# Kernel optimization log

Hardware: AMD Instinct MI355X
Metric: run time of the kernel (lower is better)

Reference implementation:

```python
import jax, jax.numpy as jnp
import numpy as np

DIM = 1024
HEADS = 16
HEAD_DIM = DIM // HEADS
MLP_HID = 4 * DIM
LN_EPS = 1e-5


def layer_norm(x, g, b):
    mu = jnp.mean(x, axis=-1, keepdims=True)
    var = jnp.mean((x - mu) ** 2, axis=-1, keepdims=True)
    return (x - mu) * jax.lax.rsqrt(var + LN_EPS) * g + b


def setup_inputs() -> dict:
    key = jax.random.key(0)
    ks = jax.random.split(key, 8)
    s = 0.02
    return {
        "x": jax.random.normal(ks[0], (8, 1024, DIM), dtype=jnp.float32),
        "attention_mask": jnp.ones((8, 1024), dtype=jnp.int32),
        "ln1_g": jnp.ones((DIM,), jnp.float32),
        "ln1_b": jnp.zeros((DIM,), jnp.float32),
        "qkv_w": jax.random.normal(ks[1], (3 * DIM, DIM), jnp.float32) * s,
        "proj_w": jax.random.normal(ks[2], (DIM, DIM), jnp.float32) * s,
        "proj_b": jnp.zeros((DIM,), jnp.float32),
        "ln2_g": jnp.ones((DIM,), jnp.float32),
        "ln2_b": jnp.zeros((DIM,), jnp.float32),
        "fc1_w": jax.random.normal(ks[3], (MLP_HID, DIM), jnp.float32) * s,
        "fc1_b": jnp.zeros((MLP_HID,), jnp.float32),
        "fc2_w": jax.random.normal(ks[4], (DIM, MLP_HID), jnp.float32) * s,
        "fc2_b": jnp.zeros((DIM,), jnp.float32),
    }


def reference(x, attention_mask, ln1_g, ln1_b, qkv_w, proj_w, proj_b,
              ln2_g, ln2_b, fc1_w, fc1_b, fc2_w, fc2_b):
    B, N, C = x.shape
    scale = HEAD_DIM ** -0.5

    # --- attention branch ---
    h = layer_norm(x, ln1_g, ln1_b)
    qkv = h @ qkv_w.T                       # [B,N,3C] (no qkv bias)
    qkv = qkv.reshape(B, N, 3, HEADS, HEAD_DIM).transpose(2, 0, 3, 1, 4)
    q, k, v = qkv[0], qkv[1], qkv[2]        # each [B,H,N,Dh]
    attn = jnp.einsum('bhnd,bhmd->bhnm', q, k) * scale
    mask = (attention_mask == 0)[:, None, None, :]  # [B,1,1,N]
    attn = jnp.where(mask, -jnp.inf, attn)
    attn = jax.nn.softmax(attn, axis=-1)
    out = jnp.einsum('bhnm,bhmd->bhnd', attn, v)
    out = out.transpose(0, 2, 1, 3).reshape(B, N, C)
    out = out @ proj_w.T + proj_b
    x = x + out

    # --- MLP branch ---
    h = layer_norm(x, ln2_g, ln2_b)
    h = jax.nn.gelu(h @ fc1_w.T + fc1_b, approximate=False)
    h = h @ fc2_w.T + fc2_b
    return x + h
```

## Files before the change

kernel.cpp:

```cpp
#include <hip/hip_runtime.h>
#include <hip/hip_bf16.h>
#include <stdint.h>
#include <math.h>

#define DIMC 1024
#define SEQ 1024
#define NBATCH 8
#define NHEADS 16
#define HDIM 64
#define MLPHID 4096
#define NROWS (NBATCH*SEQ)

typedef __attribute__((ext_vector_type(8))) short short8;
typedef __attribute__((ext_vector_type(4))) float f32x4;
typedef __attribute__((ext_vector_type(16))) float f32x16;
typedef __attribute__((ext_vector_type(4))) unsigned int u32x4;

__device__ __forceinline__ short f2bf(float f) {
  union { float f; uint32_t u; } x; x.f = f;
  uint32_t r = (x.u + 0x7FFFu + ((x.u >> 16) & 1u)) >> 16;
  return (short)r;
}

__device__ __forceinline__ unsigned int cvtpk(float lo, float hi_) {
  unsigned int r;
  asm("v_cvt_pk_bf16_f32 %0, %1, %2" : "=v"(r) : "v"(lo), "v"(hi_));
  return r;
}

__device__ __forceinline__ float gelu_f(float v) {
  const float t = v * v;
  const float p = fmaf(t, 0.044715f, 1.0f);
  const float e = __builtin_amdgcn_exp2f(2.3022082f * v * p);
  return v - v * __builtin_amdgcn_rcpf(e + 1.0f);
}

__device__ __forceinline__ f32x4 mfma16(short8 a, short8 b, f32x4 c) {
  return __builtin_amdgcn_mfma_f32_16x16x32_bf16(a, b, c, 0, 0, 0);
}
__device__ __forceinline__ f32x16 mfma32(short8 a, short8 b, f32x16 c) {
  return __builtin_amdgcn_mfma_f32_32x32x16_bf16(a, b, c, 0, 0, 0);
}

__device__ __forceinline__ void gload16(const void* g, void* l) {
  __builtin_amdgcn_global_load_lds(
      (const __attribute__((address_space(1))) uint32_t*)g,
      (__attribute__((address_space(3))) uint32_t*)l, 16, 0, 0);
}

__global__ __launch_bounds__(256)
void f2bw_kernel(const float* __restrict__ w0, const float* __restrict__ w1,
                 const float* __restrict__ w2, const float* __restrict__ w3,
                 short* __restrict__ o0, short* __restrict__ o1,
                 short* __restrict__ o2, short* __restrict__ o3) {
  const int i = blockIdx.x * 256 + threadIdx.x;
  const float4* src;
  short4* dst;
  if (i < 786432)       { src = (const float4*)w0 + i;             dst = (short4*)o0 + i; }
  else if (i < 1048576) { src = (const float4*)w1 + (i - 786432);  dst = (short4*)o1 + (i - 786432); }
  else if (i < 2097152) { src = (const float4*)w2 + (i - 1048576); dst = (short4*)o2 + (i - 1048576); }
  else                  { src = (const float4*)w3 + (i - 2097152); dst = (short4*)o3 + (i - 2097152); }
  const float4 v = *src;
  short4 o;
  o.x = f2bf(v.x); o.y = f2bf(v.y); o.z = f2bf(v.z); o.w = f2bf(v.w);
  *dst = o;
}

__global__ __launch_bounds__(256)
void ln_kernel(const float* __restrict__ x, const float* __restrict__ g,
               const float* __restrict__ beta, short* __restrict__ out) {
  const int row = blockIdx.x;
  const int tid = threadIdx.x;
  const float4 v = ((const float4*)(x + (size_t)row * DIMC))[tid];
  float s = v.x + v.y + v.z + v.w;
  float q = v.x*v.x + v.y*v.y + v.z*v.z + v.w*v.w;
#pragma unroll
  for (int o = 32; o > 0; o >>= 1) { s += __shfl_down(s, o); q += __shfl_down(q, o); }
  __shared__ float rs[4], rq[4];
  const int lane = tid & 63, w = tid >> 6;
  if (lane == 0) { rs[w] = s; rq[w] = q; }
  __syncthreads();
  s = rs[0] + rs[1] + rs[2] + rs[3];
  q = rq[0] + rq[1] + rq[2] + rq[3];
  const float mean = s * (1.0f / DIMC);
  const float var = q * (1.0f / DIMC) - mean * mean;
  const float rstd = rsqrtf(var + 1e-5f);
  const float4 gv = ((const float4*)g)[tid];
  const float4 bv = ((const float4*)beta)[tid];
  short4 o4;
  o4.x = f2bf((v.x - mean) * rstd * gv.x + bv.x);
  o4.y = f2bf((v.y - mean) * rstd * gv.y + bv.y);
  o4.z = f2bf((v.z - mean) * rstd * gv.z + bv.z);
  o4.w = f2bf((v.w - mean) * rstd * gv.w + bv.w);
  ((short4*)(out + (size_t)row * DIMC))[tid] = o4;
}

#define NOVM ((void)0)
#define NOST ((void)0)
#define VMC4 asm volatile("s_waitcnt vmcnt(4)" ::: "memory")
#define VMC2 asm volatile("s_waitcnt vmcnt(2)" ::: "memory")

#define SA(DB, H, T) \
  gload16(sA0 + (H)*hstep + (size_t)(T)*64, stb + ((DB)*4 + (H))*16384); \
  gload16(sA1 + (H)*hstep + (size_t)(T)*64, stb + ((DB)*4 + (H))*16384 + 8192)

#define SB(DB, H, T) \
  gload16(sB0 + (H)*hstep + (size_t)(T)*64, stb + ((DB)*4 + 2 + (H))*16384); \
  gload16(sB1 + (H)*hstep + (size_t)(T)*64, stb + ((DB)*4 + 2 + (H))*16384 + 8192)

#define PH(DB, QA, QB, LDA, LDB, STAGE, VM) \
  do { \
    if (LDA) { \
      _Pragma("unroll") \
      for (int mi = 0; mi < 4; ++mi) { \
        _Pragma("unroll") \
        for (int ks = 0; ks < 2; ++ks) \
          af[mi][ks] = *(const short8*)(ard##DB + (((QA)*4 + mi)*2 + ks)*1024); \
      } \
    } \
    if (LDB) { \
      _Pragma("unroll") \
      for (int ni = 0; ni < 2; ++ni) { \
        _Pragma("unroll") \
        for (int ks = 0; ks < 2; ++ks) \
          bfv[QB][ni][ks] = *(const short8*)(brd##DB + (((QB)*2 + ni)*2 + ks)*1024); \
      } \
    } \
    STAGE; \
    __builtin_amdgcn_s_barrier(); \
    asm volatile("s_waitcnt lgkmcnt(0)" ::: "memory"); \
    __builtin_amdgcn_sched_barrier(0); \
    __builtin_amdgcn_s_setprio(1); \
    _Pragma("unroll") \
    for (int ks = 0; ks < 2; ++ks) { \
      _Pragma("unroll") \
      for (int mi = 0; mi < 4; ++mi) { \
        _Pragma("unroll") \
        for (int ni = 0; ni < 2; ++ni) \
          acc[(QA)*4 + mi][(QB)*2 + ni] = \
            mfma16(af[mi][ks], bfv[QB][ni][ks], acc[(QA)*4 + mi][(QB)*2 + ni]); \
      } \
    } \
    __builtin_amdgcn_s_setprio(0); \
    VM; \
    __builtin_amdgcn_s_barrier(); \
  } while (0)

template<bool BIAS, bool GELU, bool RESID, bool OBF16>
__global__ __launch_bounds__(512)
void gemm8p(const short* __restrict__ A, const short* __restrict__ W,
            const float* __restrict__ bias, const float* __restrict__ resid,
            float* __restrict__ outF, short* __restrict__ outB,
            int M, int N, int K, int ntl, int mt8)
{
  __shared__ __align__(16) char lsm[131072];
  const int tid = threadIdx.x;
  const int lane = tid & 63;
  const int w = tid >> 6;
  const int wm = w >> 2;
  const int wn = w & 3;
  const int fr = lane & 15;
  const int fko = (lane >> 4) << 3;

  const int bid = blockIdx.x;
  const int xcd = bid & 7, l = bid >> 3;
  const int bm = (xcd * mt8 + l / ntl) << 8;
  const int bn = (l % ntl) << 8;

  int row_[2], kk_[2];
#pragma unroll
  for (int j = 0; j < 2; ++j) {
    const int s = j * 8 + (tid >> 6);
    const int r16 = (tid & 63) >> 2;
    const int cb = ((tid & 3) << 4) ^ (((tid >> 5) & 1) << 5);
    row_[j] = (s >> 1) * 16 + r16;
    kk_[j]  = (s & 1) * 32 + (cb >> 1);
  }
  const short* sA0 = A + (size_t)(bm + row_[0]) * K + kk_[0];
  const short* sA1 = A + (size_t)(bm + row_[1]) * K + kk_[1];
  const short* sB0 = W + (size_t)(bn + row_[0]) * K + kk_[0];
  const short* sB1 = W + (size_t)(bn + row_[1]) * K + kk_[1];
  const size_t hstep = (size_t)128 * K;
  char* stb = lsm + tid * 16;

  const int lofs = fr * 64 + ((fko << 1) ^ (((fr >> 3) & 1) << 5));
  const char* ard0 = lsm + wm * 16384 + lofs;
  const char* brd0 = lsm + 32768 + (wn >> 1) * 16384 + (wn & 1) * 8192 + lofs;
  const char* ard1 = ard0 + 65536;
  const char* brd1 = brd0 + 65536;

  short8 af[4][2];
  short8 bfv[2][2][2];
  f32x4 acc[8][4] = {};

  SA(0, 0, 0); SA(0, 1, 0);
  SB(0, 0, 0); SB(0, 1, 0);
  SB(1, 0, 1); SB(1, 1, 1);
  VMC4;
  __builtin_amdgcn_s_barrier();

  const int nk = K >> 6;
  const int nit = nk >> 1;
  const int tmask = nk - 1;
  for (int it = 0; it < nit; ++it) {
    const int t1 = 2 * it + 1;
    const int t2 = (2 * it + 2) & tmask;
    const int t3 = (2 * it + 3) & tmask;
    PH(0, 0, 0, 1, 1, SA(1, 0, t1), NOVM);
    PH(0, 0, 1, 0, 1, SA(1, 1, t1), NOVM);
    PH(0, 1, 1, 1, 0, SB(0, 0, t2), NOVM);
    PH(0, 1, 0, 0, 0, SB(0, 1, t2), VMC4);
    PH(1, 0, 0, 1, 1, SA(0, 0, t2), NOVM);
    PH(1, 0, 1, 0, 1, SA(0, 1, t2), NOVM);
    PH(1, 1, 1, 1, 0, SB(1, 0, t3), NOVM);
    PH(1, 1, 0, 0, 0, SB(1, 1, t3), VMC4);
  }

  asm volatile("s_waitcnt vmcnt(0)" ::: "memory");
  __builtin_amdgcn_s_barrier();

  const int orow0 = bm + wm * 128 + ((lane >> 4) << 2);
  const int ocol0 = bn + wn * 64 + fr;
#pragma unroll
  for (int mi = 0; mi < 8; ++mi) {
#pragma unroll
    for (int r = 0; r < 4; ++r) {
      const int row = orow0 + mi * 16 + r;
      const size_t base = (size_t)row * N;
#pragma unroll
      for (int ni = 0; ni < 4; ++ni) {
        const int col = ocol0 + ni * 16;
        float v = acc[mi][ni][r];
        if (BIAS) v += bias[col];
        if (GELU) v = gelu_f(v);
        if (RESID) v += resid[base + col];
        if (OBF16) outB[base + col] = f2bf(v);
        else       outF[base + col] = v;
      }
    }
  }
}

#define SA2(DB, H, T) \
  gload16(sA0 + (H)*hstep + (size_t)(T)*64, stb + ((DB)*3 + (H))*16384); \
  gload16(sA1 + (H)*hstep + (size_t)(T)*64, stb + ((DB)*3 + (H))*16384 + 8192)

#define SB2(DB, T) \
  gload16(sB0 + (size_t)(T)*64, stb + ((DB)*3 + 2)*16384); \
  gload16(sB1 + (size_t)(T)*64, stb + ((DB)*3 + 2)*16384 + 8192)

#define PH2(DB, QA, QB, LDA, LDB, STAGE, VM) \
  do { \
    if (LDA) { \
      _Pragma("unroll") \
      for (int i = 0; i < 2; ++i) { \
        _Pragma("unroll") \
        for (int ks = 0; ks < 2; ++ks) \
          af[i][ks] = *(const short8*)(ard##DB + (((QA)*2 + i)*2 + ks)*1024); \
      } \
    } \
    if (LDB) { \
      _Pragma("unroll") \
      for (int jn = 0; jn < 2; ++jn) { \
        _Pragma("unroll") \
        for (int ks = 0; ks < 2; ++ks) \
          bfv[QB][jn][ks] = *(const short8*)(brd##DB + (((QB)*2 + jn)*2 + ks)*1024); \
      } \
    } \
    STAGE; \
    __builtin_amdgcn_s_barrier(); \
    asm volatile("s_waitcnt lgkmcnt(0)" ::: "memory"); \
    __builtin_amdgcn_sched_barrier(0); \
    __builtin_amdgcn_s_setprio(1); \
    _Pragma("unroll") \
    for (int ks = 0; ks < 2; ++ks) { \
      _Pragma("unroll") \
      for (int i = 0; i < 2; ++i) { \
        _Pragma("unroll") \
        for (int jn = 0; jn < 2; ++jn) \
          acc[(QA)*2 + i][(QB)*2 + jn] = \
            mfma16(af[i][ks], bfv[QB][jn][ks], acc[(QA)*2 + i][(QB)*2 + jn]); \
      } \
    } \
    __builtin_amdgcn_s_setprio(0); \
    VM; \
    __builtin_amdgcn_s_barrier(); \
  } while (0)

template<bool BIAS, bool GELU, bool RESID, bool OBF16, bool QSCALE>
__global__ __launch_bounds__(512)
void gemm8pn(const short* __restrict__ A, const short* __restrict__ W,
             const float* __restrict__ bias, const float* __restrict__ resid,
             float* __restrict__ outF, short* __restrict__ outB,
             int M, int N, int K, int ntl, int mt8)
{
  __shared__ __align__(16) char lsm[98304];
  const int tid = threadIdx.x;
  const int lane = tid & 63;
  const int w = tid >> 6;
  const int wm = w >> 1;
  const int wn = w & 1;
  const int fr = lane & 15;
  const int fko = (lane >> 4) << 3;

  const int bid = blockIdx.x;
  const int xcd = bid & 7, l = bid >> 3;
  const int bm = (xcd * mt8 + l / ntl) << 8;
  const int bn = (l % ntl) << 7;

  int row_[2], kk_[2];
#pragma unroll
  for (int j = 0; j < 2; ++j) {
    const int s = j * 8 + (tid >> 6);
    const int r16 = (tid & 63) >> 2;
    const int cb = ((tid & 3) << 4) ^ (((tid >> 5) & 1) << 5);
    row_[j] = (s >> 1) * 16 + r16;
    kk_[j]  = (s & 1) * 32 + (cb >> 1);
  }
  const short* sA0 = A + (size_t)(bm + row_[0]) * K + kk_[0];
  const short* sA1 = A + (size_t)(bm + row_[1]) * K + kk_[1];
  const short* sB0 = W + (size_t)(bn + row_[0]) * K + kk_[0];
  const short* sB1 = W + (size_t)(bn + row_[1]) * K + kk_[1];
  const size_t hstep = (size_t)128 * K;
  char* stb = lsm + tid * 16;

  const int lofs = fr * 64 + ((fko << 1) ^ (((fr >> 3) & 1) << 5));
  const char* ard0 = lsm + (wm >> 1) * 16384 + (wm & 1) * 8192 + lofs;
  const char* brd0 = lsm + 32768 + wn * 8192 + lofs;
  const char* ard1 = ard0 + 49152;
  const char* brd1 = brd0 + 49152;

  short8 af[2][2];
  short8 bfv[2][2][2];
  f32x4 acc[4][4] = {};

  SA2(0, 0, 0); SA2(0, 1, 0); SB2(0, 0);
  SB2(1, 1);
  VMC2;
  __builtin_amdgcn_s_barrier();

  const int nk = K >> 6;
  const int nit = nk >> 1;
  const int tmask = nk - 1;
  for (int it = 0; it < nit; ++it) {
    const int t1 = 2 * it + 1;
    const int t2 = (2 * it + 2) & tmask;
    const int t3 = (2 * it + 3) & tmask;
    PH2(0, 0, 0, 1, 1, SA2(1, 0, t1), NOVM);
    PH2(0, 0, 1, 0, 1, SA2(1, 1, t1), NOVM);
    PH2(0, 1, 1, 1, 0, SB2(0, t2),    NOVM);
    PH2(0, 1, 0, 0, 0, NOST,          VMC2);
    PH2(1, 0, 0, 1, 1, SA2(0, 0, t2), NOVM);
    PH2(1, 0, 1, 0, 1, SA2(0, 1, t2), NOVM);
    PH2(1, 1, 1, 1, 0, SB2(1, t3),    NOVM);
    PH2(1, 1, 0, 0, 0, NOST,          VMC2);
  }

  asm volatile("s_waitcnt vmcnt(0)" ::: "memory");
  __builtin_amdgcn_s_barrier();

  const int orow0 = bm + wm * 64 + ((lane >> 4) << 2);
  const int ocol0 = bn + wn * 64 + fr;
#pragma unroll
  for (int mi = 0; mi < 4; ++mi) {
#pragma unroll
    for (int r = 0; r < 4; ++r) {
      const int row = orow0 + mi * 16 + r;
      const size_t base = (size_t)row * N;
#pragma unroll
      for (int ni = 0; ni < 4; ++ni) {
        const int col = ocol0 + ni * 16;
        float v = acc[mi][ni][r];
        if (BIAS) v += bias[col];
        if (GELU) v = gelu_f(v);
        if (QSCALE) v *= (col < 1024 ? 0.18033688f : 1.0f);
        if (RESID) v += resid[base + col];
        if (OBF16) outB[base + col] = f2bf(v);
        else       outF[base + col] = v;
      }
    }
  }
}

__global__ __launch_bounds__(256)
void attn_kernel(const short* __restrict__ qkv, const int* __restrict__ amask,
                 short* __restrict__ out)
{
  __shared__ __align__(16) char lsm[36864];
  char* lsK = lsm;
  char* lsV = lsm + 16384;
  int* lmask = (int*)(lsm + 32768);
  __shared__ int anym;

  const int tid = threadIdx.x;
  const int lane = tid & 63;
  const int w = tid >> 6;
  const int l31 = lane & 31;
  const int hi = lane >> 5;
  const int swz = (l31 & 7) << 4;

  const int bid = blockIdx.x;
  const int swzb = ((bid & 7) << 7) | (bid >> 3);
  const int qt = swzb & 7;
  const int h = (swzb >> 3) & 15;
  const int b = swzb >> 7;
  const size_t rowbase = (size_t)b * SEQ;
  const short* qkvB = qkv + rowbase * 3072 + h * 64;

  const int4 mv = ((const int4*)(amask + b * SEQ))[tid];
  if (tid == 0) anym = 0;
  ((int4*)lmask)[tid] = mv;
  __syncthreads();
  if ((mv.x & mv.y & mv.z & mv.w) == 0) atomicOr(&anym, 1);

  const int q0 = qt * 128 + w * 32;
  const short* qptr = qkvB + (size_t)(q0 + l31) * 3072;
  short8 qf[4];
#pragma unroll
  for (int ks = 0; ks < 4; ++ks)
    qf[ks] = *(const short8*)(qptr + ks * 16 + hi * 8);

  const int krow = tid >> 3;
  const int kcc = (((tid & 7) * 16) ^ ((krow & 7) << 4)) >> 1;
  const short* gK = qkvB + 1024 + kcc;
  char* ldK = lsK + tid * 16;
  const int vr = tid & 63;
  const int vc0 = (tid >> 6) << 3;
  const short* gV = qkvB + 2048 + vc0;

  gload16(gK + (size_t)krow * 3072, ldK);
  gload16(gK + (size_t)(krow + 32) * 3072, ldK + 4096);
  {
    short8 a0 = *(const short8*)(gV + (size_t)vr * 3072);
    short8 a1 = *(const short8*)(gV + (size_t)vr * 3072 + 32);
#pragma unroll
    for (int j = 0; j < 8; ++j) {
      *(short*)(lsV + (vc0 + j) * 128 + ((2 * vr) ^ (j << 4))) = a0[j];
      *(short*)(lsV + (vc0 + 32 + j) * 128 + ((2 * vr) ^ (j << 4))) = a1[j];
    }
  }
  __syncthreads();

  f32x16 oacc[2] = {};
  float psum = 0.f;

  for (int c = 0; c < 16; ++c) {
    const int cur = c & 1;
    const char* lKc = lsK + cur * 8192;
    const char* lVc = lsV + cur * 8192;
    const bool pf = (c < 15);
    short8 vv0, vv1;
    if (pf) {
      const size_t nb_ = (size_t)(c + 1) * 64;
      char* ldKn = ldK + (cur ^ 1) * 8192;
      gload16(gK + (nb_ + krow) * 3072, ldKn);
      gload16(gK + (nb_ + krow + 32) * 3072, ldKn + 4096);
      vv0 = *(const short8*)(gV + (nb_ + vr) * 3072);
      vv1 = *(const short8*)(gV + (nb_ + vr) * 3072 + 32);
    }

    f32x16 pacc[2] = {};
    __builtin_amdgcn_s_setprio(1);
#pragma unroll
    for (int ks = 0; ks < 4; ++ks) {
#pragma unroll
      for (int s = 0; s < 2; ++s) {
        short8 kf = *(const short8*)(lKc + (s * 32 + l31) * 128 +
                                     ((ks * 32 + hi * 16) ^ swz));
        pacc[s] = mfma32(kf, qf[ks], pacc[s]);
      }
    }
    __builtin_amdgcn_s_setprio(0);

    if (pf) {
      char* lVn = lsV + (cur ^ 1) * 8192;
#pragma unroll
      for (int j = 0; j < 8; ++j) {
        *(short*)(lVn + (vc0 + j) * 128 + ((2 * vr) ^ (j << 4))) = vv0[j];
        *(short*)(lVn + (vc0 + 32 + j) * 128 + ((2 * vr) ^ (j << 4))) = vv1[j];
      }
    }

    if (anym) {
      const int kv0 = c * 64;
#pragma unroll
      for (int s = 0; s < 2; ++s)
#pragma unroll
        for (int r = 0; r < 16; ++r) {
          const int kv = kv0 + 32 * s + (r & 3) + 8 * (r >> 2) + 4 * hi;
          if (lmask[kv] == 0) pacc[s][r] = -1e30f;
        }
    }

    float pe[2][16];
#pragma unroll
    for (int s = 0; s < 2; ++s)
#pragma unroll
      for (int r = 0; r < 16; ++r) {
        const float p = __builtin_amdgcn_exp2f(pacc[s][r]);
        pe[s][r] = p;
        psum += p;
      }

    short8 pa[4];
#pragma unroll
    for (int ks = 0; ks < 4; ++ks) {
      const int sh = ks >> 1, kb = (ks & 1) << 3;
      unsigned int aa = cvtpk(pe[sh][kb + 0], pe[sh][kb + 1]);
      unsigned int bb = cvtpk(pe[sh][kb + 4], pe[sh][kb + 5]);
      unsigned int cc = cvtpk(pe[sh][kb + 2], pe[sh][kb + 3]);
      unsigned int dd = cvtpk(pe[sh][kb + 6], pe[sh][kb + 7]);
      asm volatile("v_permlane32_swap_b32 %0, %1" : "+v"(aa), "+v"(bb));
      asm volatile("v_permlane32_swap_b32 %0, %1" : "+v"(cc), "+v"(dd));
      u32x4 t;
      t[0] = aa; t[1] = cc; t[2] = bb; t[3] = dd;
      pa[ks] = __builtin_bit_cast(short8, t);
    }

    __builtin_amdgcn_s_setprio(1);
#pragma unroll
    for (int nb = 0; nb < 2; ++nb)
#pragma unroll
      for (int ks = 0; ks < 4; ++ks) {
        short8 vf = *(const short8*)(lVc + (nb * 32 + l31) * 128 +
                                     ((ks * 32 + hi * 16) ^ swz));
        oacc[nb] = mfma32(pa[ks], vf, oacc[nb]);
      }
    __builtin_amdgcn_s_setprio(0);

    __syncthreads();
  }

  const float lt = psum + __shfl_xor(psum, 32);
  const size_t orow = rowbase + q0;
#pragma unroll
  for (int r = 0; r < 16; ++r) {
    const int q = (r & 3) + 8 * (r >> 2) + 4 * hi;
    const float linv = 1.0f / __shfl(lt, q);
    short* op = out + (orow + q) * DIMC + h * 64 + l31;
    op[0]  = f2bf(oacc[0][r] * linv);
    op[32] = f2bf(oacc[1][r] * linv);
  }
}

extern "C" void kernel_launch(void* const* d_in, const int* in_sizes, int n_in,
                              void* d_out, int out_size, void* d_ws, size_t ws_size,
                              hipStream_t stream)
{
  const float* x      = (const float*)d_in[0];
  const int*   amask  = (const int*)d_in[1];
  const float* ln1_g  = (const float*)d_in[2];
  const float* ln1_b  = (const float*)d_in[3];
  const float* qkv_w  = (const float*)d_in[4];
  const float* proj_w = (const float*)d_in[5];
  const float* proj_b = (const float*)d_in[6];
  const float* ln2_g  = (const float*)d_in[7];
  const float* ln2_b  = (const float*)d_in[8];
  const float* fc1_w  = (const float*)d_in[9];
  const float* fc1_b  = (const float*)d_in[10];
  const float* fc2_w  = (const float*)d_in[11];
  const float* fc2_b  = (const float*)d_in[12];
  float* out = (float*)d_out;

  char* ws = (char*)d_ws;
  short* wqkv  = (short*)(ws);
  short* wproj = (short*)(ws + 6291456);
  short* wfc1  = (short*)(ws + 8388608);
  short* wfc2  = (short*)(ws + 16777216);
  float* x1    = (float*)(ws + 25165824);
  short* hb    = (short*)(ws + 58720256);
  short* qkvo  = (short*)(ws + 75497472);
  short* attno = (short*)(ws + 125829120);
  short* fc1o  = (short*)(ws + 75497472);

  f2bw_kernel<<<12288, 256, 0, stream>>>(qkv_w, proj_w, fc1_w, fc2_w,
                                         wqkv, wproj, wfc1, wfc2);

  ln_kernel<<<NROWS, 256, 0, stream>>>(x, ln1_g, ln1_b, hb);

  gemm8pn<false, false, false, true, true><<<768, 512, 0, stream>>>(
      hb, wqkv, nullptr, nullptr, nullptr, qkvo, NROWS, 3 * DIMC, DIMC, 24, 4);

  attn_kernel<<<1024, 256, 0, stream>>>(qkvo, amask, attno);

  gemm8pn<true, false, true, false, false><<<256, 512, 0, stream>>>(
      attno, wproj, proj_b, x, x1, nullptr, NROWS, DIMC, DIMC, 8, 4);

  ln_kernel<<<NROWS, 256, 0, stream>>>(x1, ln2_g, ln2_b, hb);

  gemm8p<true, true, false, true><<<512, 512, 0, stream>>>(
      hb, wfc1, fc1_b, nullptr, nullptr, fc1o, NROWS, MLPHID, DIMC, 16, 4);

  gemm8pn<true, false, true, false, false><<<256, 512, 0, stream>>>(
      fc1o, wfc2, fc2_b, x1, out, nullptr, NROWS, DIMC, MLPHID, 8, 4);
}
```

Before: 327.1 us.

## Deepen B-tile prefetch in gemm8pn and use it for fc1

Reworks the 256x128 GEMM pipeline so the B operand is staged into four rotating LDS buffers, prefetched several K-steps ahead. A is issued as a whole tile per stage. LDS use grows to 128KB. The fc1 GEMM moves from the 256x256 gemm8p kernel to this narrower kernel with twice the blocks, and gemm8p is removed. The aim is to hide global-load latency and improve load balance, at the cost of more LDS (lower occupancy) and more A reloads for fc1.

Result: slower. 343.9 us (+5.1%).

```diff
diff --git a/kernel.cpp b/kernel.cpp
--- a/kernel.cpp
+++ b/kernel.cpp
@@ -95,168 +95,30 @@
   ((short4*)(out + (size_t)row * DIMC))[tid] = o4;
 }
 
+
 #define NOVM ((void)0)
 #define NOST ((void)0)
 #define VMC4 asm volatile("s_waitcnt vmcnt(4)" ::: "memory")
 #define VMC2 asm volatile("s_waitcnt vmcnt(2)" ::: "memory")
 
-#define SA(DB, H, T) \
-  gload16(sA0 + (H)*hstep + (size_t)(T)*64, stb + ((DB)*4 + (H))*16384); \
-  gload16(sA1 + (H)*hstep + (size_t)(T)*64, stb + ((DB)*4 + (H))*16384 + 8192)
-
-#define SB(DB, H, T) \
-  gload16(sB0 + (H)*hstep + (size_t)(T)*64, stb + ((DB)*4 + 2 + (H))*16384); \
-  gload16(sB1 + (H)*hstep + (size_t)(T)*64, stb + ((DB)*4 + 2 + (H))*16384 + 8192)
-
-#define PH(DB, QA, QB, LDA, LDB, STAGE, VM) \
-  do { \
-    if (LDA) { \
-      _Pragma("unroll") \
-      for (int mi = 0; mi < 4; ++mi) { \
-        _Pragma("unroll") \
-        for (int ks = 0; ks < 2; ++ks) \
-          af[mi][ks] = *(const short8*)(ard##DB + (((QA)*4 + mi)*2 + ks)*1024); \
-      } \
-    } \
-    if (LDB) { \
-      _Pragma("unroll") \
-      for (int ni = 0; ni < 2; ++ni) { \
-        _Pragma("unroll") \
-        for (int ks = 0; ks < 2; ++ks) \
-          bfv[QB][ni][ks] = *(const short8*)(brd##DB + (((QB)*2 + ni)*2 + ks)*1024); \
-      } \
-    } \
-    STAGE; \
-    __builtin_amdgcn_s_barrier(); \
-    asm volatile("s_waitcnt lgkmcnt(0)" ::: "memory"); \
-    __builtin_amdgcn_sched_barrier(0); \
-    __builtin_amdgcn_s_setprio(1); \
-    _Pragma("unroll") \
-    for (int ks = 0; ks < 2; ++ks) { \
-      _Pragma("unroll") \
-      for (int mi = 0; mi < 4; ++mi) { \
-        _Pragma("unroll") \
-        for (int ni = 0; ni < 2; ++ni) \
-          acc[(QA)*4 + mi][(QB)*2 + ni] = \
-            mfma16(af[mi][ks], bfv[QB][ni][ks], acc[(QA)*4 + mi][(QB)*2 + ni]); \
-      } \
-    } \
-    __builtin_amdgcn_s_setprio(0); \
-    VM; \
-    __builtin_amdgcn_s_barrier(); \
-  } while (0)
-
-template<bool BIAS, bool GELU, bool RESID, bool OBF16>
-__global__ __launch_bounds__(512)
-void gemm8p(const short* __restrict__ A, const short* __restrict__ W,
-            const float* __restrict__ bias, const float* __restrict__ resid,
-            float* __restrict__ outF, short* __restrict__ outB,
-            int M, int N, int K, int ntl, int mt8)
-{
-  __shared__ __align__(16) char lsm[131072];
-  const int tid = threadIdx.x;
-  const int lane = tid & 63;
-  const int w = tid >> 6;
-  const int wm = w >> 2;
-  const int wn = w & 3;
-  const int fr = lane & 15;
-  const int fko = (lane >> 4) << 3;
-
-  const int bid = blockIdx.x;
-  const int xcd = bid & 7, l = bid >> 3;
-  const int bm = (xcd * mt8 + l / ntl) << 8;
-  const int bn = (l % ntl) << 8;
-
-  int row_[2], kk_[2];
-#pragma unroll
-  for (int j = 0; j < 2; ++j) {
-    const int s = j * 8 + (tid >> 6);
-    const int r16 = (tid & 63) >> 2;
-    const int cb = ((tid & 3) << 4) ^ (((tid >> 5) & 1) << 5);
-    row_[j] = (s >> 1) * 16 + r16;
-    kk_[j]  = (s & 1) * 32 + (cb >> 1);
-  }
-  const short* sA0 = A + (size_t)(bm + row_[0]) * K + kk_[0];
-  const short* sA1 = A + (size_t)(bm + row_[1]) * K + kk_[1];
-  const short* sB0 = W + (size_t)(bn + row_[0]) * K + kk_[0];
-  const short* sB1 = W + (size_t)(bn + row_[1]) * K + kk_[1];
-  const size_t hstep = (size_t)128 * K;
-  char* stb = lsm + tid * 16;
-
-  const int lofs = fr * 64 + ((fko << 1) ^ (((fr >> 3) & 1) << 5));
-  const char* ard0 = lsm + wm * 16384 + lofs;
-  const char* brd0 = lsm + 32768 + (wn >> 1) * 16384 + (wn & 1) * 8192 + lofs;
-  const char* ard1 = ard0 + 65536;
-  const char* brd1 = brd0 + 65536;
-
-  short8 af[4][2];
-  short8 bfv[2][2][2];
-  f32x4 acc[8][4] = {};
-
-  SA(0, 0, 0); SA(0, 1, 0);
-  SB(0, 0, 0); SB(0, 1, 0);
-  SB(1, 0, 1); SB(1, 1, 1);
-  VMC4;
-  __builtin_amdgcn_s_barrier();
-
-  const int nk = K >> 6;
-  const int nit = nk >> 1;
-  const int tmask = nk - 1;
-  for (int it = 0; it < nit; ++it) {
-    const int t1 = 2 * it + 1;
-    const int t2 = (2 * it + 2) & tmask;
-    const int t3 = (2 * it + 3) & tmask;
-    PH(0, 0, 0, 1, 1, SA(1, 0, t1), NOVM);
-    PH(0, 0, 1, 0, 1, SA(1, 1, t1), NOVM);
-    PH(0, 1, 1, 1, 0, SB(0, 0, t2), NOVM);
-    PH(0, 1, 0, 0, 0, SB(0, 1, t2), VMC4);
-    PH(1, 0, 0, 1, 1, SA(0, 0, t2), NOVM);
-    PH(1, 0, 1, 0, 1, SA(0, 1, t2), NOVM);
-    PH(1, 1, 1, 1, 0, SB(1, 0, t3), NOVM);
-    PH(1, 1, 0, 0, 0, SB(1, 1, t3), VMC4);
-  }
-
-  asm volatile("s_waitcnt vmcnt(0)" ::: "memory");
-  __builtin_amdgcn_s_barrier();
-
-  const int orow0 = bm + wm * 128 + ((lane >> 4) << 2);
-  const int ocol0 = bn + wn * 64 + fr;
-#pragma unroll
-  for (int mi = 0; mi < 8; ++mi) {
-#pragma unroll
-    for (int r = 0; r < 4; ++r) {
-      const int row = orow0 + mi * 16 + r;
-      const size_t base = (size_t)row * N;
-#pragma unroll
-      for (int ni = 0; ni < 4; ++ni) {
-        const int col = ocol0 + ni * 16;
-        float v = acc[mi][ni][r];
-        if (BIAS) v += bias[col];
-        if (GELU) v = gelu_f(v);
-        if (RESID) v += resid[base + col];
-        if (OBF16) outB[base + col] = f2bf(v);
-        else       outF[base + col] = v;
-      }
-    }
-  }
-}
-
-#define SA2(DB, H, T) \
-  gload16(sA0 + (H)*hstep + (size_t)(T)*64, stb + ((DB)*3 + (H))*16384); \
-  gload16(sA1 + (H)*hstep + (size_t)(T)*64, stb + ((DB)*3 + (H))*16384 + 8192)
-
-#define SB2(DB, T) \
-  gload16(sB0 + (size_t)(T)*64, stb + ((DB)*3 + 2)*16384); \
-  gload16(sB1 + (size_t)(T)*64, stb + ((DB)*3 + 2)*16384 + 8192)
-
-#define PH2(DB, QA, QB, LDA, LDB, STAGE, VM) \
+#define SAQ(DB, T) \
+  gload16(sA0 + (size_t)(T)*64,         stbA + (DB)*32768); \
+  gload16(sA1 + (size_t)(T)*64,         stbA + (DB)*32768 + 8192); \
+  gload16(sA0 + hstep + (size_t)(T)*64, stbA + (DB)*32768 + 16384); \
+  gload16(sA1 + hstep + (size_t)(T)*64, stbA + (DB)*32768 + 24576)
+
+#define SBQ(ST, T) \
+  gload16(sB0 + (size_t)(T)*64, (ST)); \
+  gload16(sB1 + (size_t)(T)*64, (ST) + 8192)
+
+#define PH2(ARD, BRD, QA, QB, LDA, LDB, STAGE, VM) \
   do { \
     if (LDA) { \
       _Pragma("unroll") \
       for (int i = 0; i < 2; ++i) { \
         _Pragma("unroll") \
         for (int ks = 0; ks < 2; ++ks) \
-          af[i][ks] = *(const short8*)(ard##DB + (((QA)*2 + i)*2 + ks)*1024); \
+          af[i][ks] = *(const short8*)((ARD) + (((QA)*2 + i)*2 + ks)*1024); \
       } \
     } \
     if (LDB) { \
@@ -264,7 +126,7 @@
       for (int jn = 0; jn < 2; ++jn) { \
         _Pragma("unroll") \
         for (int ks = 0; ks < 2; ++ks) \
-          bfv[QB][jn][ks] = *(const short8*)(brd##DB + (((QB)*2 + jn)*2 + ks)*1024); \
+          bfv[QB][jn][ks] = *(const short8*)((BRD) + (((QB)*2 + jn)*2 + ks)*1024); \
       } \
     } \
     STAGE; \
@@ -294,7 +156,7 @@
              float* __restrict__ outF, short* __restrict__ outB,
              int M, int N, int K, int ntl, int mt8)
 {
-  __shared__ __align__(16) char lsm[98304];
+  __shared__ __align__(16) char lsm[131072];
   const int tid = threadIdx.x;
   const int lane = tid & 63;
   const int w = tid >> 6;
@@ -322,38 +184,52 @@
   const short* sB0 = W + (size_t)(bn + row_[0]) * K + kk_[0];
   const short* sB1 = W + (size_t)(bn + row_[1]) * K + kk_[1];
   const size_t hstep = (size_t)128 * K;
-  char* stb = lsm + tid * 16;
+  char* stbA = lsm + tid * 16;
 
   const int lofs = fr * 64 + ((fko << 1) ^ (((fr >> 3) & 1) << 5));
   const char* ard0 = lsm + (wm >> 1) * 16384 + (wm & 1) * 8192 + lofs;
-  const char* brd0 = lsm + 32768 + wn * 8192 + lofs;
-  const char* ard1 = ard0 + 49152;
-  const char* brd1 = brd0 + 49152;
+  const char* ard1 = ard0 + 32768;
+  const char* brdE  = lsm + 65536 + 0 * 16384 + wn * 8192 + lofs;
+  const char* brdO  = lsm + 65536 + 1 * 16384 + wn * 8192 + lofs;
+  const char* brdEx = lsm + 65536 + 2 * 16384 + wn * 8192 + lofs;
+  const char* brdOx = lsm + 65536 + 3 * 16384 + wn * 8192 + lofs;
+  char* stE  = lsm + 65536 + 0 * 16384 + tid * 16;
+  char* stO  = lsm + 65536 + 1 * 16384 + tid * 16;
+  char* stEx = lsm + 65536 + 2 * 16384 + tid * 16;
+  char* stOx = lsm + 65536 + 3 * 16384 + tid * 16;
 
   short8 af[2][2];
   short8 bfv[2][2][2];
   f32x4 acc[4][4] = {};
 
-  SA2(0, 0, 0); SA2(0, 1, 0); SB2(0, 0);
-  SB2(1, 1);
-  VMC2;
-  __builtin_amdgcn_s_barrier();
-
   const int nk = K >> 6;
   const int nit = nk >> 1;
   const int tmask = nk - 1;
+
+  SAQ(0, 0);
+  SBQ(stE, 0); SBQ(stO, 1); SBQ(stEx, 2); SBQ(stOx, 3 & tmask);
+  VMC4;
+  __builtin_amdgcn_s_barrier();
+
   for (int it = 0; it < nit; ++it) {
-    const int t1 = 2 * it + 1;
-    const int t2 = (2 * it + 2) & tmask;
-    const int t3 = (2 * it + 3) & tmask;
-    PH2(0, 0, 0, 1, 1, SA2(1, 0, t1), NOVM);
-    PH2(0, 0, 1, 0, 1, SA2(1, 1, t1), NOVM);
-    PH2(0, 1, 1, 1, 0, SB2(0, t2),    NOVM);
-    PH2(0, 1, 0, 0, 0, NOST,          VMC2);
-    PH2(1, 0, 0, 1, 1, SA2(0, 0, t2), NOVM);
-    PH2(1, 0, 1, 0, 1, SA2(0, 1, t2), NOVM);
-    PH2(1, 1, 1, 1, 0, SB2(1, t3),    NOVM);
-    PH2(1, 1, 0, 0, 0, NOST,          VMC2);
+    const int t1  = 2 * it + 1;
+    const int t2  = (2 * it + 2) & tmask;
+    const int tb0 = (2 * it + 4) & tmask;
+    const int tb1 = (2 * it + 5) & tmask;
+    PH2(ard0, brdE, 0, 0, 1, 1, SAQ(1, t1),    NOVM);
+    PH2(ard0, brdE, 0, 1, 0, 1, SBQ(stE, tb0), NOVM);
+    PH2(ard0, brdE, 1, 1, 1, 0, NOST,          NOVM);
+    PH2(ard0, brdE, 1, 0, 0, 0, NOST,          VMC2);
+    PH2(ard1, brdO, 0, 0, 1, 1, SAQ(0, t2),    NOVM);
+    PH2(ard1, brdO, 0, 1, 0, 1, SBQ(stO, tb1), NOVM);
+    PH2(ard1, brdO, 1, 1, 1, 0, NOST,          NOVM);
+    PH2(ard1, brdO, 1, 0, 0, 0, NOST,          VMC2);
+    const char* tp;
+    tp = brdE; brdE = brdEx; brdEx = tp;
+    tp = brdO; brdO = brdOx; brdOx = tp;
+    char* tq;
+    tq = stE; stE = stEx; stEx = tq;
+    tq = stO; stO = stOx; stOx = tq;
   }
 
   asm volatile("s_waitcnt vmcnt(0)" ::: "memory");
@@ -588,8 +464,8 @@
 
   ln_kernel<<<NROWS, 256, 0, stream>>>(x1, ln2_g, ln2_b, hb);
 
-  gemm8p<true, true, false, true><<<512, 512, 0, stream>>>(
-      hb, wfc1, fc1_b, nullptr, nullptr, fc1o, NROWS, MLPHID, DIMC, 16, 4);
+  gemm8pn<true, true, false, true, false><<<1024, 512, 0, stream>>>(
+      hb, wfc1, fc1_b, nullptr, nullptr, fc1o, NROWS, MLPHID, DIMC, 32, 4);
 
   gemm8pn<true, false, true, false, false><<<256, 512, 0, stream>>>(
       fc1o, wfc2, fc2_b, x1, out, nullptr, NROWS, DIMC, MLPHID, 8, 4);
```

## Add half-height 128x128 GEMM kernel for proj and fc2 to double grid size

Applied to the files above, without the earlier changes.

Adds a new GEMM variant (gemm8ph) that uses 128x128 output tiles with 8 waves, each computing 32x64, and a triple-buffered B stage. It replaces the 256-block launches for the projection and fc2 GEMMs with 512-block launches. This is meant to fix under-occupancy of the 256 CUs, which the N=1024 GEMMs leave idle with large tiles. In exchange it lowers per-block data reuse, so A and W tiles are reloaded more often and global/LDS traffic per flop rises.

Result: no change. 328.4 us (+0.4%).

```diff
diff --git a/kernel.cpp b/kernel.cpp
--- a/kernel.cpp
+++ b/kernel.cpp
@@ -95,6 +95,7 @@
   ((short4*)(out + (size_t)row * DIMC))[tid] = o4;
 }
 
+
 #define NOVM ((void)0)
 #define NOST ((void)0)
 #define VMC4 asm volatile("s_waitcnt vmcnt(4)" ::: "memory")
@@ -374,6 +375,149 @@
         if (BIAS) v += bias[col];
         if (GELU) v = gelu_f(v);
         if (QSCALE) v *= (col < 1024 ? 0.18033688f : 1.0f);
+        if (RESID) v += resid[base + col];
+        if (OBF16) outB[base + col] = f2bf(v);
+        else       outF[base + col] = v;
+      }
+    }
+  }
+}
+
+#define SAH(DB, T) \
+  gload16(sA0 + (size_t)(T)*64, stb + (DB)*16384); \
+  gload16(sA1 + (size_t)(T)*64, stb + (DB)*16384 + 8192)
+
+#define SBH(ST, T) \
+  gload16(sB0 + (size_t)(T)*64, (ST)); \
+  gload16(sB1 + (size_t)(T)*64, (ST) + 8192)
+
+#define PHH(ARD, BRD, QB, LDA, STAGE, VM) \
+  do { \
+    if (LDA) { \
+      _Pragma("unroll") \
+      for (int mi = 0; mi < 2; ++mi) { \
+        _Pragma("unroll") \
+        for (int ks = 0; ks < 2; ++ks) \
+          af[mi][ks] = *(const short8*)((ARD) + (mi*2 + ks)*1024); \
+      } \
+    } \
+    _Pragma("unroll") \
+    for (int jn = 0; jn < 2; ++jn) { \
+      _Pragma("unroll") \
+      for (int ks = 0; ks < 2; ++ks) \
+        bq[jn][ks] = *(const short8*)((BRD) + (((QB)*2 + jn)*2 + ks)*1024); \
+    } \
+    STAGE; \
+    __builtin_amdgcn_s_barrier(); \
+    asm volatile("s_waitcnt lgkmcnt(0)" ::: "memory"); \
+    __builtin_amdgcn_sched_barrier(0); \
+    __builtin_amdgcn_s_setprio(1); \
+    _Pragma("unroll") \
+    for (int ks = 0; ks < 2; ++ks) { \
+      _Pragma("unroll") \
+      for (int mi = 0; mi < 2; ++mi) { \
+        _Pragma("unroll") \
+        for (int jn = 0; jn < 2; ++jn) \
+          acc[mi][(QB)*2 + jn] = \
+            mfma16(af[mi][ks], bq[jn][ks], acc[mi][(QB)*2 + jn]); \
+      } \
+    } \
+    __builtin_amdgcn_s_setprio(0); \
+    VM; \
+    __builtin_amdgcn_s_barrier(); \
+  } while (0)
+
+template<bool BIAS, bool GELU, bool RESID, bool OBF16>
+__global__ __launch_bounds__(512, 4)
+void gemm8ph(const short* __restrict__ A, const short* __restrict__ W,
+             const float* __restrict__ bias, const float* __restrict__ resid,
+             float* __restrict__ outF, short* __restrict__ outB,
+             int M, int N, int K, int ntl, int mt8)
+{
+  __shared__ __align__(16) char lsm[81920];
+  const int tid = threadIdx.x;
+  const int lane = tid & 63;
+  const int w = tid >> 6;
+  const int wm = w >> 1;
+  const int wn = w & 1;
+  const int fr = lane & 15;
+  const int fko = (lane >> 4) << 3;
+
+  const int bid = blockIdx.x;
+  const int xcd = bid & 7, l = bid >> 3;
+  const int bm = (xcd * mt8 + l / ntl) << 7;
+  const int bn = (l % ntl) << 7;
+
+  int row_[2], kk_[2];
+#pragma unroll
+  for (int j = 0; j < 2; ++j) {
+    const int s = j * 8 + (tid >> 6);
+    const int r16 = (tid & 63) >> 2;
+    const int cb = ((tid & 3) << 4) ^ (((tid >> 5) & 1) << 5);
+    row_[j] = (s >> 1) * 16 + r16;
+    kk_[j]  = (s & 1) * 32 + (cb >> 1);
+  }
+  const short* sA0 = A + (size_t)(bm + row_[0]) * K + kk_[0];
+  const short* sA1 = A + (size_t)(bm + row_[1]) * K + kk_[1];
+  const short* sB0 = W + (size_t)(bn + row_[0]) * K + kk_[0];
+  const short* sB1 = W + (size_t)(bn + row_[1]) * K + kk_[1];
+  char* stb = lsm + tid * 16;
+
+  const int lofs = fr * 64 + ((fko << 1) ^ (((fr >> 3) & 1) << 5));
+  const char* ard0 = lsm + wm * 4096 + lofs;
+  const char* ard1 = ard0 + 16384;
+  const char* bp0r = lsm + 32768 + 0 * 16384 + wn * 8192 + lofs;
+  const char* bp1r = lsm + 32768 + 1 * 16384 + wn * 8192 + lofs;
+  const char* bp2r = lsm + 32768 + 2 * 16384 + wn * 8192 + lofs;
+  char* bp0s = lsm + 32768 + 0 * 16384 + tid * 16;
+  char* bp1s = lsm + 32768 + 1 * 16384 + tid * 16;
+  char* bp2s = lsm + 32768 + 2 * 16384 + tid * 16;
+
+  short8 af[2][2];
+  short8 bq[2][2];
+  f32x4 acc[2][4] = {};
+
+  const int nk = K >> 6;
+  const int nit = nk >> 1;
+  const int tmask = nk - 1;
+
+  SBH(bp0s, 0);
+  SAH(0, 0);
+  SBH(bp1s, 1);
+  SAH(1, 1);
+  VMC4;
+  __builtin_amdgcn_s_barrier();
+
+  for (int it = 0; it < nit; ++it) {
+    const int t2 = (2 * it + 2) & tmask;
+    const int t3 = (2 * it + 3) & tmask;
+    PHH(ard0, bp0r, 0, 1, SBH(bp2s, t2), NOVM);
+    PHH(ard0, bp0r, 1, 0, SAH(0, t2),    VMC4);
+    PHH(ard1, bp1r, 0, 1, SBH(bp0s, t3), NOVM);
+    PHH(ard1, bp1r, 1, 0, SAH(1, t3),    VMC4);
+    const char* tr;
+    tr = bp0r; bp0r = bp2r; bp2r = bp1r; bp1r = tr;
+    char* ts;
+    ts = bp0s; bp0s = bp2s; bp2s = bp1s; bp1s = ts;
+  }
+
+  asm volatile("s_waitcnt vmcnt(0)" ::: "memory");
+  __builtin_amdgcn_s_barrier();
+
+  const int orow0 = bm + wm * 32 + ((lane >> 4) << 2);
+  const int ocol0 = bn + wn * 64 + fr;
+#pragma unroll
+  for (int mi = 0; mi < 2; ++mi) {
+#pragma unroll
+    for (int r = 0; r < 4; ++r) {
+      const int row = orow0 + mi * 16 + r;
+      const size_t base = (size_t)row * N;
+#pragma unroll
+      for (int ni = 0; ni < 4; ++ni) {
+        const int col = ocol0 + ni * 16;
+        float v = acc[mi][ni][r];
+        if (BIAS) v += bias[col];
+        if (GELU) v = gelu_f(v);
         if (RESID) v += resid[base + col];
         if (OBF16) outB[base + col] = f2bf(v);
         else       outF[base + col] = v;
@@ -583,14 +727,14 @@
 
   attn_kernel<<<1024, 256, 0, stream>>>(qkvo, amask, attno);
 
-  gemm8pn<true, false, true, false, false><<<256, 512, 0, stream>>>(
-      attno, wproj, proj_b, x, x1, nullptr, NROWS, DIMC, DIMC, 8, 4);
+  gemm8ph<true, false, true, false><<<512, 512, 0, stream>>>(
+      attno, wproj, proj_b, x, x1, nullptr, NROWS, DIMC, DIMC, 8, 8);
 
   ln_kernel<<<NROWS, 256, 0, stream>>>(x1, ln2_g, ln2_b, hb);
 
   gemm8p<true, true, false, true><<<512, 512, 0, stream>>>(
       hb, wfc1, fc1_b, nullptr, nullptr, fc1o, NROWS, MLPHID, DIMC, 16, 4);
 
-  gemm8pn<true, false, true, false, false><<<256, 512, 0, stream>>>(
-      fc1o, wfc2, fc2_b, x1, out, nullptr, NROWS, DIMC, MLPHID, 8, 4);
-}
+  gemm8ph<true, false, true, false><<<512, 512, 0, stream>>>(
+      fc1o, wfc2, fc2_b, x1, out, nullptr, NROWS, DIMC, MLPHID, 8, 8);
+}
```
